# Optimization experiments

Hardware: AMD Instinct MI355X
Metric: run time of the kernel (lower is better)

The kernel has to match this reference:

```python
import jax, jax.numpy as jnp
import numpy as np

RES = 4096
MAX_VAL = 1.0
COST_SCALE = 0.01
WIDTH = 11
N_ITERS = 20


def setup_inputs() -> dict:
    key = jax.random.key(0)
    k1, k2, k3, k4 = jax.random.split(key, 4)
    x = jax.random.uniform(k1, (RES, RES), jnp.float32)
    bt = jax.random.randint(k2, (RES, RES), 1, 3).astype(jnp.float32)
    sparse = (jax.random.uniform(k4, (RES, RES)) < 0.01).astype(jnp.float32)
    boundary_types = bt * sparse
    boundary_conditions = jax.random.uniform(k3, (RES, RES), jnp.float32) * MAX_VAL
    C = COST_SCALE * jnp.ones((RES, RES), jnp.float32)
    return {"x": x, "boundary_types": boundary_types,
            "boundary_conditions": boundary_conditions, "C": C}


def _neighbor_avg(V):
    # 5-point Jacobi stencil average with edge-replicate boundary handling
    Vp = jnp.pad(V, 1, mode='edge')
    return 0.25 * (Vp[:-2, 1:-1] + Vp[2:, 1:-1] + Vp[1:-1, :-2] + Vp[1:-1, 2:])


def reference(x, boundary_types, boundary_conditions, C):
    obj = boundary_types > 0
    V0 = jnp.where(obj, boundary_conditions, x)
    C_pos = jax.nn.relu(C)

    # dilate object boundary values with a uniform width x width box filter
    objects_bounds = boundary_conditions * (boundary_types == 1) * (boundary_conditions > 0)
    w = jnp.full((1, 1, WIDTH, WIDTH), 1.0 / (WIDTH * WIDTH), jnp.float32)
    extra = jax.lax.conv_general_dilated(
        objects_bounds[None, None], w, window_strides=(1, 1), padding='SAME')[0, 0]
    extra = extra * (boundary_types == 0)
    Cc = C_pos + extra  # effective cost field, shape (RES, RES)

    interior = boundary_types == 0

    def step(V, _):
        Vn = jnp.where(interior, _neighbor_avg(V) + Cc, boundary_conditions)
        return Vn, None

    V, _ = jax.lax.scan(step, V0, None, length=N_ITERS)

    out = jnp.where(V >= MAX_VAL, 0.95 * MAX_VAL, V)
    out = jnp.where(obj, boundary_conditions, out)
    return (out, C_pos)
```

## Files before the change

kernel.cpp:

```cpp
#include <hip/hip_runtime.h>
#include <cstdint>

#define RES 4096
#define N_CELLS (RES*RES)

#define T_STEPS 5
#define OW 64
#define OH 64
#define HALO_V 5
#define HALO_H 8
#define IW (OW + 2*HALO_H)
#define IH (OH + 2*HALO_V)
#define NF4 (IW/4)
#define NSLOT (NF4*IH)
#define NTHR 512
#define LDSW IW
#define BUFSZ (IH*LDSW + 8)
#define K2_LIM (NSLOT - 2*NTHR)

__device__ __forceinline__ float4 jcalc(const float* buf,
                                        int lo, int gr, int gc, uint4 pk)
{
    const float4 ctr = *(const float4*)(buf + lo);
    const int upo = (gr == 0)     ? lo : lo - LDSW;
    const int dno = (gr == RES-1) ? lo : lo + LDSW;
    const float4 up  = *(const float4*)(buf + upo);
    const float4 dn  = *(const float4*)(buf + dno);
    const float4 lfq = *(const float4*)(buf + (lo - 4));
    const float4 rtq = *(const float4*)(buf + (lo + 4));
    const float lf = (gc == 0)         ? ctr.x : lfq.w;
    const float rt = (gc + 3 == RES-1) ? ctr.w : rtq.x;
    float4 nv;
    {   const float m = __uint_as_float(pk.x & 0x7fffffffu);
        const float a = 0.25f*(up.x + dn.x + lf    + ctr.y) + m;
        nv.x = (pk.x >> 31) ? m : a; }
    {   const float m = __uint_as_float(pk.y & 0x7fffffffu);
        const float a = 0.25f*(up.y + dn.y + ctr.x + ctr.z) + m;
        nv.y = (pk.y >> 31) ? m : a; }
    {   const float m = __uint_as_float(pk.z & 0x7fffffffu);
        const float a = 0.25f*(up.z + dn.z + ctr.y + ctr.w) + m;
        nv.z = (pk.z >> 31) ? m : a; }
    {   const float m = __uint_as_float(pk.w & 0x7fffffffu);
        const float a = 0.25f*(up.w + dn.w + ctr.z + rt   ) + m;
        nv.w = (pk.w >> 31) ? m : a; }
    return nv;
}

__device__ __forceinline__ void stage_slot(const float* __restrict__ Vin,
                                           const uint32_t* __restrict__ packed,
                                           float* buf,
                                           int idx, int r0, int c0,
                                           int& lo, int& gr, int& gc, uint4& pk)
{
    const int lrow  = idx / NF4;
    const int lcol4 = idx - lrow * NF4;
    gr = r0 - HALO_V + lrow;
    gc = c0 - HALO_H + lcol4 * 4;
    lo = lrow * LDSW + lcol4 * 4;
    float4 vv; uint4 pp;
    const int rr = gr < 0 ? 0 : (gr > RES-1 ? RES-1 : gr);
    if (gc >= 0 && gc + 3 <= RES-1) {
        vv = *(const float4*)(Vin    + (size_t)rr * RES + gc);
        pp = *(const uint4*) (packed + (size_t)rr * RES + gc);
    } else {
#pragma unroll
        for (int e = 0; e < 4; ++e) {
            int cc = gc + e; cc = cc < 0 ? 0 : (cc > RES-1 ? RES-1 : cc);
            ((float*)&vv)[e]    = Vin   [(size_t)rr * RES + cc];
            ((uint32_t*)&pp)[e] = packed[(size_t)rr * RES + cc];
        }
    }
    *(float4*)(buf + lo) = vv;
    pk = pp;
}

template<int FINAL>
__global__ __launch_bounds__(NTHR, 8) void lap_fused(
    const float* __restrict__ Vin, const uint32_t* __restrict__ packed,
    float* __restrict__ Vout)
{
    __shared__ float lds_raw[BUFSZ];
    float* buf = lds_raw + 4;
    const int tid = threadIdx.x;
    const int r0 = blockIdx.y * OH;
    const int c0 = blockIdx.x * OW;

    int lo0, gr0, gc0;  uint4 pk0;
    int lo1, gr1, gc1;  uint4 pk1;
    int lo2 = 0, gr2 = 0, gc2 = 0;  uint4 pk2 = {0u,0u,0u,0u};

    stage_slot(Vin, packed, buf, tid,            r0, c0, lo0, gr0, gc0, pk0);
    stage_slot(Vin, packed, buf, tid + NTHR,     r0, c0, lo1, gr1, gc1, pk1);
    if (tid < K2_LIM)
        stage_slot(Vin, packed, buf, tid + 2*NTHR, r0, c0, lo2, gr2, gc2, pk2);
    __syncthreads();

    for (int s = 1; s < T_STEPS; ++s) {
        const int rlo = (r0 == 0)        ? 0   : (r0 - HALO_V + s);
        const int rhi = (r0 + OH == RES) ? RES : (r0 + OH + HALO_V - s);
        const bool a0 = (gr0 >= rlo) && (gr0 < rhi);
        const bool a1 = (gr1 >= rlo) && (gr1 < rhi);
        const bool a2 = (tid < K2_LIM) && (gr2 >= rlo) && (gr2 < rhi);
        float4 nv0, nv1, nv2;
        if (a0) nv0 = jcalc(buf, lo0, gr0, gc0, pk0);
        if (a1) nv1 = jcalc(buf, lo1, gr1, gc1, pk1);
        if (a2) nv2 = jcalc(buf, lo2, gr2, gc2, pk2);
        __syncthreads();
        if (a0) *(float4*)(buf + lo0) = nv0;
        if (a1) *(float4*)(buf + lo1) = nv1;
        if (a2) *(float4*)(buf + lo2) = nv2;
        __syncthreads();
    }

#define FINAL_SLOT(LO, GR, GC, PK, ACT)                                        \
    if ((ACT) && (GR) >= r0 && (GR) < r0 + OH && (GC) >= c0 && (GC) < c0 + OW) {\
        float4 o = jcalc(buf, (LO), (GR), (GC), (PK));                         \
        if (FINAL) {                                                           \
            o.x = ((PK).x >> 31) ? o.x : (o.x >= 1.0f ? 0.95f : o.x);          \
            o.y = ((PK).y >> 31) ? o.y : (o.y >= 1.0f ? 0.95f : o.y);          \
            o.z = ((PK).z >> 31) ? o.z : (o.z >= 1.0f ? 0.95f : o.z);          \
            o.w = ((PK).w >> 31) ? o.w : (o.w >= 1.0f ? 0.95f : o.w);          \
        }                                                                      \
        *(float4*)(Vout + (size_t)(GR) * RES + (GC)) = o;                      \
    }
    FINAL_SLOT(lo0, gr0, gc0, pk0, true)
    FINAL_SLOT(lo1, gr1, gc1, pk1, true)
    FINAL_SLOT(lo2, gr2, gc2, pk2, tid < K2_LIM)
#undef FINAL_SLOT
}

#define PB_OW 64
#define PB_OH 64
#define PB_HH 8
#define PB_HV 5
#define PB_IW (PB_OW + 2*PB_HH)
#define PB_IH (PB_OH + 2*PB_HV)
#define PB_NF4 (PB_IW/4)
#define PB_NSLOT (PB_NF4*PB_IH)
#define PB_THR 512
#define PB_LDSW 84
#define PB_HLDSW 68

__global__ __launch_bounds__(PB_THR, 6) void lap_precompute(
    const float* __restrict__ x, const float* __restrict__ bt,
    const float* __restrict__ bc, const float* __restrict__ C,
    float* __restrict__ V0, uint32_t* __restrict__ packed)
{
    __shared__ float ob[PB_IH * PB_LDSW];
    __shared__ float hs[PB_IH * PB_HLDSW];
    const int tid = threadIdx.x;
    const int r0 = blockIdx.y * PB_OH, c0 = blockIdx.x * PB_OW;

    for (int idx = tid; idx < PB_NSLOT; idx += PB_THR) {
        const int lrow = idx / PB_NF4;
        const int lcol4 = idx - lrow * PB_NF4;
        const int gr = r0 - PB_HV + lrow;
        const int gc = c0 - PB_HH + lcol4 * 4;
        float4 o = {0.f,0.f,0.f,0.f};
        if (gr >= 0 && gr < RES) {
            if (gc >= 0 && gc + 3 < RES) {
                const float4 b = *(const float4*)(bt + (size_t)gr*RES + gc);
                const float4 w = *(const float4*)(bc + (size_t)gr*RES + gc);
                o.x = (b.x == 1.f && w.x > 0.f) ? w.x : 0.f;
                o.y = (b.y == 1.f && w.y > 0.f) ? w.y : 0.f;
                o.z = (b.z == 1.f && w.z > 0.f) ? w.z : 0.f;
                o.w = (b.w == 1.f && w.w > 0.f) ? w.w : 0.f;
            } else {
#pragma unroll
                for (int e = 0; e < 4; ++e) {
                    const int cc = gc + e;
                    if (cc >= 0 && cc < RES) {
                        const float b = bt[(size_t)gr*RES + cc];
                        const float w = bc[(size_t)gr*RES + cc];
                        ((float*)&o)[e] = (b == 1.f && w > 0.f) ? w : 0.f;
                    }
                }
            }
        }
        *(float4*)(&ob[lrow*PB_LDSW + lcol4*4]) = o;
    }
    __syncthreads();

    for (int idx = tid; idx < PB_IH * 16; idx += PB_THR) {
        const int lrow = idx >> 4;
        const int j4 = (idx & 15) << 2;
        const float* row = &ob[lrow * PB_LDSW];
        const float4 a0 = *(const float4*)(row + j4);
        const float4 a1 = *(const float4*)(row + j4 + 4);
        const float4 a2 = *(const float4*)(row + j4 + 8);
        const float4 a3 = *(const float4*)(row + j4 + 12);
        const float4 a4 = *(const float4*)(row + j4 + 16);
        const float common = a1.z + a1.w + a2.x + a2.y + a2.z + a2.w + a3.x + a3.y;
        float4 s;
        s.x = common + a0.w + a1.x + a1.y;
        s.y = common + a1.x + a1.y + a3.z;
        s.z = common + a1.y + a3.z + a3.w;
        s.w = common + a3.z + a3.w + a4.x;
        *(float4*)(&hs[lrow * PB_HLDSW + j4]) = s;
    }
    __syncthreads();

    for (int idx = tid; idx < PB_OH * 16; idx += PB_THR) {
        const int i = idx >> 4;
        const int j4 = (idx & 15) << 2;
        float sx=0.f, sy=0.f, sz=0.f, sw=0.f;
#pragma unroll
        for (int d = 0; d < 11; ++d) {
            const float4 h = *(const float4*)(&hs[(i + d) * PB_HLDSW + j4]);
            sx += h.x; sy += h.y; sz += h.z; sw += h.w;
        }
        const int gr = r0 + i, gc = c0 + j4;
        const size_t g = (size_t)gr * RES + gc;
        const float4 xx  = *(const float4*)(x  + g);
        const float4 cc  = *(const float4*)(C  + g);
        const float4 btv = *(const float4*)(bt + g);
        const float4 bcv = *(const float4*)(bc + g);
        float4 v0; uint4 pko;
        const float es[4] = {sx, sy, sz, sw};
#pragma unroll
        for (int e = 0; e < 4; ++e) {
            const float cpos = fmaxf(((const float*)&cc)[e], 0.f);
            const bool interior = (((const float*)&btv)[e] == 0.0f);
            const float Cc = cpos + es[e] * (1.0f / 121.0f);
            const float bce = ((const float*)&bcv)[e];
            ((uint32_t*)&pko)[e] = interior ? __float_as_uint(Cc)
                                           : (__float_as_uint(bce) | 0x80000000u);
            ((float*)&v0)[e] = interior ? ((const float*)&xx)[e] : bce;
        }
        *(uint4*)(packed + g) = pko;
        *(float4*)(V0 + g) = v0;
    }
}

__global__ __launch_bounds__(256) void lap_cpos(
    const float* __restrict__ C, float* __restrict__ out2)
{
    const int idx = (blockIdx.x * 256 + threadIdx.x) * 4;
    const float4 c = *(const float4*)(C + idx);
    float4 o;
    o.x = fmaxf(c.x, 0.f); o.y = fmaxf(c.y, 0.f);
    o.z = fmaxf(c.z, 0.f); o.w = fmaxf(c.w, 0.f);
    *(float4*)(out2 + idx) = o;
}

extern "C" void kernel_launch(void* const* d_in, const int* in_sizes, int n_in,
                              void* d_out, int out_size, void* d_ws, size_t ws_size,
                              hipStream_t stream) {
    const float* x  = (const float*)d_in[0];
    const float* bt = (const float*)d_in[1];
    const float* bc = (const float*)d_in[2];
    const float* C  = (const float*)d_in[3];

    float*    out1   = (float*)d_out;
    uint32_t* packed = (uint32_t*)((float*)d_out + N_CELLS);
    float*    vb     = (float*)d_ws;

    dim3 gP(RES / PB_OW, RES / PB_OH);
    lap_precompute<<<gP, PB_THR, 0, stream>>>(x, bt, bc, C, out1, packed);

    dim3 gF(RES / OW, RES / OH);
    lap_fused<0><<<gF, NTHR, 0, stream>>>(out1, packed, vb);
    lap_fused<0><<<gF, NTHR, 0, stream>>>(vb,   packed, out1);
    lap_fused<0><<<gF, NTHR, 0, stream>>>(out1, packed, vb);
    lap_fused<1><<<gF, NTHR, 0, stream>>>(vb,   packed, out1);

    lap_cpos<<<N_CELLS / 1024, 256, 0, stream>>>(C, (float*)d_out + N_CELLS);
}
```

Before: 594.9 us.

## Replace LDS-tiled 5-step Jacobi with register-resident 10-step temporal blocking

Replaces the four LDS-tiled launches of five fused Jacobi steps with two launches of ten steps each, using 1024-thread blocks on 128x128 tiles with a 12-cell halo. Each thread keeps a 4-row by float4 patch in registers, takes left and right neighbours via wavefront shuffles, and exchanges only the top and bottom rows through a small double-buffered LDS array. The aim is to halve global round trips and cut LDS traffic and barriers per step. The cost is more redundant halo work, since only 104x104 of each 128x128 tile is written, and higher register pressure per thread.

```diff
diff --git a/kernel.cpp b/kernel.cpp
--- a/kernel.cpp
+++ b/kernel.cpp
@@ -4,129 +4,108 @@
 #define RES 4096
 #define N_CELLS (RES*RES)
 
-#define T_STEPS 5
-#define OW 64
-#define OH 64
-#define HALO_V 5
-#define HALO_H 8
-#define IW (OW + 2*HALO_H)
-#define IH (OH + 2*HALO_V)
-#define NF4 (IW/4)
-#define NSLOT (NF4*IH)
-#define NTHR 512
-#define LDSW IW
-#define BUFSZ (IH*LDSW + 8)
-#define K2_LIM (NSLOT - 2*NTHR)
-
-__device__ __forceinline__ float4 jcalc(const float* buf,
-                                        int lo, int gr, int gc, uint4 pk)
-{
-    const float4 ctr = *(const float4*)(buf + lo);
-    const int upo = (gr == 0)     ? lo : lo - LDSW;
-    const int dno = (gr == RES-1) ? lo : lo + LDSW;
-    const float4 up  = *(const float4*)(buf + upo);
-    const float4 dn  = *(const float4*)(buf + dno);
-    const float4 lfq = *(const float4*)(buf + (lo - 4));
-    const float4 rtq = *(const float4*)(buf + (lo + 4));
-    const float lf = (gc == 0)         ? ctr.x : lfq.w;
-    const float rt = (gc + 3 == RES-1) ? ctr.w : rtq.x;
+#define MT_OW 104
+#define MT_OH 104
+#define MT_HH 12
+#define MT_HV 12
+#define MT_IW 128
+#define MT_IH 128
+#define MT_GRID 40
+
+__device__ __forceinline__ float4 jrow(float4 up, float4 dn, const float4 cur,
+                                       const uint4 pk, const int gr, const int gc)
+{
+    float lf = __shfl_up(cur.w, 1);
+    float rt = __shfl_down(cur.x, 1);
+    lf = (gc == 0)         ? cur.x : lf;
+    rt = (gc + 3 == RES-1) ? cur.w : rt;
+    if (gr <= 0)       up = cur;
+    if (gr >= RES - 1) dn = cur;
     float4 nv;
     {   const float m = __uint_as_float(pk.x & 0x7fffffffu);
-        const float a = 0.25f*(up.x + dn.x + lf    + ctr.y) + m;
-        nv.x = (pk.x >> 31) ? m : a; }
+        nv.x = (pk.x >> 31) ? m : 0.25f*(up.x + dn.x + lf    + cur.y) + m; }
     {   const float m = __uint_as_float(pk.y & 0x7fffffffu);
-        const float a = 0.25f*(up.y + dn.y + ctr.x + ctr.z) + m;
-        nv.y = (pk.y >> 31) ? m : a; }
+        nv.y = (pk.y >> 31) ? m : 0.25f*(up.y + dn.y + cur.x + cur.z) + m; }
     {   const float m = __uint_as_float(pk.z & 0x7fffffffu);
-        const float a = 0.25f*(up.z + dn.z + ctr.y + ctr.w) + m;
-        nv.z = (pk.z >> 31) ? m : a; }
+        nv.z = (pk.z >> 31) ? m : 0.25f*(up.z + dn.z + cur.y + cur.w) + m; }
     {   const float m = __uint_as_float(pk.w & 0x7fffffffu);
-        const float a = 0.25f*(up.w + dn.w + ctr.z + rt   ) + m;
-        nv.w = (pk.w >> 31) ? m : a; }
+        nv.w = (pk.w >> 31) ? m : 0.25f*(up.w + dn.w + cur.z + rt   ) + m; }
     return nv;
 }
 
-__device__ __forceinline__ void stage_slot(const float* __restrict__ Vin,
-                                           const uint32_t* __restrict__ packed,
-                                           float* buf,
-                                           int idx, int r0, int c0,
-                                           int& lo, int& gr, int& gc, uint4& pk)
-{
-    const int lrow  = idx / NF4;
-    const int lcol4 = idx - lrow * NF4;
-    gr = r0 - HALO_V + lrow;
-    gc = c0 - HALO_H + lcol4 * 4;
-    lo = lrow * LDSW + lcol4 * 4;
-    float4 vv; uint4 pp;
-    const int rr = gr < 0 ? 0 : (gr > RES-1 ? RES-1 : gr);
-    if (gc >= 0 && gc + 3 <= RES-1) {
-        vv = *(const float4*)(Vin    + (size_t)rr * RES + gc);
-        pp = *(const uint4*) (packed + (size_t)rr * RES + gc);
-    } else {
-#pragma unroll
-        for (int e = 0; e < 4; ++e) {
-            int cc = gc + e; cc = cc < 0 ? 0 : (cc > RES-1 ? RES-1 : cc);
-            ((float*)&vv)[e]    = Vin   [(size_t)rr * RES + cc];
-            ((uint32_t*)&pp)[e] = packed[(size_t)rr * RES + cc];
-        }
-    }
-    *(float4*)(buf + lo) = vv;
-    pk = pp;
-}
-
-template<int FINAL>
-__global__ __launch_bounds__(NTHR, 8) void lap_fused(
+template<int T, int FINAL>
+__global__ __launch_bounds__(1024, 8) void lap_march(
     const float* __restrict__ Vin, const uint32_t* __restrict__ packed,
     float* __restrict__ Vout)
 {
-    __shared__ float lds_raw[BUFSZ];
-    float* buf = lds_raw + 4;
-    const int tid = threadIdx.x;
-    const int r0 = blockIdx.y * OH;
-    const int c0 = blockIdx.x * OW;
-
-    int lo0, gr0, gc0;  uint4 pk0;
-    int lo1, gr1, gc1;  uint4 pk1;
-    int lo2 = 0, gr2 = 0, gc2 = 0;  uint4 pk2 = {0u,0u,0u,0u};
-
-    stage_slot(Vin, packed, buf, tid,            r0, c0, lo0, gr0, gc0, pk0);
-    stage_slot(Vin, packed, buf, tid + NTHR,     r0, c0, lo1, gr1, gc1, pk1);
-    if (tid < K2_LIM)
-        stage_slot(Vin, packed, buf, tid + 2*NTHR, r0, c0, lo2, gr2, gc2, pk2);
-    __syncthreads();
-
-    for (int s = 1; s < T_STEPS; ++s) {
-        const int rlo = (r0 == 0)        ? 0   : (r0 - HALO_V + s);
-        const int rhi = (r0 + OH == RES) ? RES : (r0 + OH + HALO_V - s);
-        const bool a0 = (gr0 >= rlo) && (gr0 < rhi);
-        const bool a1 = (gr1 >= rlo) && (gr1 < rhi);
-        const bool a2 = (tid < K2_LIM) && (gr2 >= rlo) && (gr2 < rhi);
-        float4 nv0, nv1, nv2;
-        if (a0) nv0 = jcalc(buf, lo0, gr0, gc0, pk0);
-        if (a1) nv1 = jcalc(buf, lo1, gr1, gc1, pk1);
-        if (a2) nv2 = jcalc(buf, lo2, gr2, gc2, pk2);
+    __shared__ float4 bnd[2][32][2][32];
+    const int tid   = threadIdx.x;
+    const int c     = tid & 31;
+    const int strip = tid >> 5;
+    const int o0 = blockIdx.x * MT_OW;
+    const int r0 = blockIdx.y * MT_OH;
+    const int gc  = o0 - MT_HH + 4*c;
+    const int grb = r0 - MT_HV + 4*strip;
+
+    float4 v0, v1, v2, v3;  uint4 p0, p1, p2, p3;
+    {
+        auto loadrow = [&](int gr, float4& vv, uint4& pp) {
+            const int rr = gr < 0 ? 0 : (gr > RES-1 ? RES-1 : gr);
+            const size_t base = (size_t)rr * RES;
+            if ((unsigned)gc < (unsigned)RES) {
+                vv = *(const float4*)(Vin + base + gc);
+                pp = *(const uint4*)(packed + base + gc);
+            } else {
+#pragma unroll
+                for (int e = 0; e < 4; ++e) {
+                    int cc = gc + e; cc = cc < 0 ? 0 : (cc > RES-1 ? RES-1 : cc);
+                    ((float*)&vv)[e]    = Vin   [base + cc];
+                    ((uint32_t*)&pp)[e] = packed[base + cc];
+                }
+            }
+        };
+        loadrow(grb + 0, v0, p0);
+        loadrow(grb + 1, v1, p1);
+        loadrow(grb + 2, v2, p2);
+        loadrow(grb + 3, v3, p3);
+    }
+
+    for (int s = 1; s <= T; ++s) {
+        const int par = s & 1;
+        bnd[par][strip][0][c] = v0;
+        bnd[par][strip][1][c] = v3;
         __syncthreads();
-        if (a0) *(float4*)(buf + lo0) = nv0;
-        if (a1) *(float4*)(buf + lo1) = nv1;
-        if (a2) *(float4*)(buf + lo2) = nv2;
-        __syncthreads();
-    }
-
-#define FINAL_SLOT(LO, GR, GC, PK, ACT)                                        \
-    if ((ACT) && (GR) >= r0 && (GR) < r0 + OH && (GC) >= c0 && (GC) < c0 + OW) {\
-        float4 o = jcalc(buf, (LO), (GR), (GC), (PK));                         \
-        if (FINAL) {                                                           \
-            o.x = ((PK).x >> 31) ? o.x : (o.x >= 1.0f ? 0.95f : o.x);          \
-            o.y = ((PK).y >> 31) ? o.y : (o.y >= 1.0f ? 0.95f : o.y);          \
-            o.z = ((PK).z >> 31) ? o.z : (o.z >= 1.0f ? 0.95f : o.z);          \
-            o.w = ((PK).w >> 31) ? o.w : (o.w >= 1.0f ? 0.95f : o.w);          \
-        }                                                                      \
-        *(float4*)(Vout + (size_t)(GR) * RES + (GC)) = o;                      \
-    }
-    FINAL_SLOT(lo0, gr0, gc0, pk0, true)
-    FINAL_SLOT(lo1, gr1, gc1, pk1, true)
-    FINAL_SLOT(lo2, gr2, gc2, pk2, tid < K2_LIM)
-#undef FINAL_SLOT
+        const int sa = strip > 0  ? strip - 1 : 0;
+        const int sb = strip < 31 ? strip + 1 : 31;
+        const float4 above = bnd[par][sa][1][c];
+        const float4 below = bnd[par][sb][0][c];
+        const float4 t0 = v0, t1 = v1, t2 = v2;
+        v0 = jrow(above, v1,    v0, p0, grb + 0, gc);
+        v1 = jrow(t0,    v2,    v1, p1, grb + 1, gc);
+        v2 = jrow(t1,    v3,    v2, p2, grb + 2, gc);
+        v3 = jrow(t2,    below, v3, p3, grb + 3, gc);
+    }
+
+    if (c >= 3 && c < 29 && gc < RES) {
+#define STORE_ROW(J, VV, PP)                                                   \
+        {   const int gr = grb + (J);                                          \
+            if (gr >= r0 && gr < r0 + MT_OH && gr < RES) {                     \
+                float4 o = VV;                                                 \
+                if (FINAL) {                                                   \
+                    o.x = ((PP).x >> 31) ? o.x : (o.x >= 1.0f ? 0.95f : o.x);  \
+                    o.y = ((PP).y >> 31) ? o.y : (o.y >= 1.0f ? 0.95f : o.y);  \
+                    o.z = ((PP).z >> 31) ? o.z : (o.z >= 1.0f ? 0.95f : o.z);  \
+                    o.w = ((PP).w >> 31) ? o.w : (o.w >= 1.0f ? 0.95f : o.w);  \
+                }                                                              \
+                *(float4*)(Vout + (size_t)gr * RES + gc) = o;                  \
+            }                                                                  \
+        }
+        STORE_ROW(0, v0, p0)
+        STORE_ROW(1, v1, p1)
+        STORE_ROW(2, v2, p2)
+        STORE_ROW(3, v3, p3)
+#undef STORE_ROW
+    }
 }
 
 #define PB_OW 64
@@ -258,11 +237,9 @@
     dim3 gP(RES / PB_OW, RES / PB_OH);
     lap_precompute<<<gP, PB_THR, 0, stream>>>(x, bt, bc, C, out1, packed);
 
-    dim3 gF(RES / OW, RES / OH);
-    lap_fused<0><<<gF, NTHR, 0, stream>>>(out1, packed, vb);
-    lap_fused<0><<<gF, NTHR, 0, stream>>>(vb,   packed, out1);
-    lap_fused<0><<<gF, NTHR, 0, stream>>>(out1, packed, vb);
-    lap_fused<1><<<gF, NTHR, 0, stream>>>(vb,   packed, out1);
+    dim3 gM(MT_GRID, MT_GRID);
+    lap_march<10, 0><<<gM, 1024, 0, stream>>>(out1, packed, vb);
+    lap_march<10, 1><<<gM, 1024, 0, stream>>>(vb, packed, out1);
 
     lap_cpos<<<N_CELLS / 1024, 256, 0, stream>>>(C, (float*)d_out + N_CELLS);
 }
```

New measurement: 548.8 us. -7.7%, faster.
